# Performance work log

Measured on AMD Instinct MI355X. Metric: run time of the kernel, lower is better.

## Reference

```python
import jax, jax.numpy as jnp
import numpy as np

N, E, IN, H, C, T = 50000, 800000, 128, 64, 64, 2
F1, FO1 = H, H // T   # conv1: per-tower in/out feats
F2, FO2 = H, C // T   # conv2
STD_EPS = 1e-5
BN_EPS = 1e-5


def setup_inputs() -> dict:
    key = jax.random.key(0)
    ks = jax.random.split(key, 12)
    rn = lambda k, s, sc=0.05: jax.random.normal(k, s, jnp.float32) * sc
    return {
        "x": jax.random.normal(ks[0], (N, IN), jnp.float32),
        "embed_W": rn(ks[1], (IN, H)),
        "embed_b": jnp.zeros((H,), jnp.float32),
        "pre_W1": rn(ks[2], (T, 2 * F1, F1)),
        "pre_b1": jnp.zeros((T, F1), jnp.float32),
        "post_W1": rn(ks[3], (T, 13 * F1, FO1)),
        "post_b1": jnp.zeros((T, FO1), jnp.float32),
        "lin_W1": rn(ks[4], (H, H)),
        "lin_b1": jnp.zeros((H,), jnp.float32),
        "bn_gamma": jnp.ones((H,), jnp.float32),
        "bn_beta": jnp.zeros((H,), jnp.float32),
        "pre_W2": rn(ks[5], (T, 2 * F2, F2)),
        "pre_b2": jnp.zeros((T, F2), jnp.float32),
        "post_W2": rn(ks[6], (T, 13 * F2, FO2)),
        "post_b2": jnp.zeros((T, FO2), jnp.float32),
        "lin_W2": rn(ks[7], (C, C)),
        "lin_b2": jnp.zeros((C,), jnp.float32),
        "src": jax.random.randint(ks[8], (E,), 0, N, jnp.int32),
        "dst": jax.random.randint(ks[9], (E,), 0, N, jnp.int32),
    }


def _pna_conv(h, src, dst, deg_raw, degc, avg_log, preW, preb, postW, postb, linW, linb):
    # h: [N, F] node feats; messages flow src -> dst, aggregated at dst.
    m = jnp.concatenate([h[dst], h[src]], axis=-1)            # [E, 2F]  (cat[x_i, x_j])
    m = jnp.einsum('ef,tfg->etg', m, preW) + preb[None]       # [E, T, F] per-tower pre-NN
    seg = lambda v: jax.ops.segment_sum(v, dst, num_segments=N)
    cnt = degc[:, None, None]                                 # clamped degree >= 1
    has = (deg_raw > 0)[:, None, None]
    mean = seg(m) / cnt                                       # [N, T, F]
    mean_sq = seg(m * m) / cnt
    mn = jnp.where(has, jax.ops.segment_min(m, dst, num_segments=N), 0.0)
    mx = jnp.where(has, jax.ops.segment_max(m, dst, num_segments=N), 0.0)
    std = jnp.sqrt(jax.nn.relu(mean_sq - mean * mean) + STD_EPS)
    agg = jnp.concatenate([mean, mn, mx, std], axis=-1)       # [N, T, 4F]
    ld = jnp.log(degc + 1.0)[:, None, None]
    out = jnp.concatenate([agg, agg * (ld / avg_log), agg * (avg_log / ld)], axis=-1)  # [N, T, 12F]
    F = h.shape[-1]
    out = jnp.concatenate([jnp.broadcast_to(h[:, None, :], (N, T, F)), out], axis=-1)  # [N, T, 13F]
    out = jnp.einsum('ntf,tfg->ntg', out, postW) + postb[None]  # [N, T, FO] per-tower post-NN
    return out.reshape(N, -1) @ linW + linb                    # final mixing Linear(out, out)


def reference(x, embed_W, embed_b, pre_W1, pre_b1, post_W1, post_b1, lin_W1, lin_b1,
              bn_gamma, bn_beta, pre_W2, pre_b2, post_W2, post_b2, lin_W2, lin_b2,
              src, dst):
    deg_raw = jax.ops.segment_sum(jnp.ones((E,), jnp.float32), dst, num_segments=N)
    degc = jnp.maximum(deg_raw, 1.0)
    avg_log = jnp.mean(jnp.log(deg_raw + 1.0))  # avg_deg['log'] from the graph's degrees
    h = x @ embed_W + embed_b
    h = _pna_conv(h, src, dst, deg_raw, degc, avg_log,
                  pre_W1, pre_b1, post_W1, post_b1, lin_W1, lin_b1)
    mu = jnp.mean(h, axis=0)
    var = jnp.mean((h - mu) ** 2, axis=0)
    h = bn_gamma * (h - mu) / jnp.sqrt(var + BN_EPS) + bn_beta
    h = jax.nn.relu(h)  # dropout is identity in eval mode
    return _pna_conv(h, src, dst, deg_raw, degc, avg_log,
                     pre_W2, pre_b2, post_W2, post_b2, lin_W2, lin_b2)
```

## Files before the change

### kernel.cpp

```cpp
#include <hip/hip_runtime.h>

#define N_NODES 50000
#define E_EDGES 800000
#define IN_F    128
#define H_F     64
#define STD_EPS 1e-5f
#define BN_EPS  1e-5f

__global__ __launch_bounds__(256) void k_hist(const int* __restrict__ dst,
                                              int* __restrict__ deg) {
  int e = blockIdx.x * 256 + threadIdx.x;
  if (e < E_EDGES) atomicAdd(&deg[dst[e]], 1);
}

__global__ __launch_bounds__(256) void k_sumlog(const int* __restrict__ deg,
                                                float* __restrict__ scalars) {
  __shared__ float red[256];
  int i = blockIdx.x * 256 + threadIdx.x;
  float v = 0.f;
  if (i < N_NODES) v = logf((float)deg[i] + 1.0f);
  red[threadIdx.x] = v; __syncthreads();
  for (int s = 128; s > 0; s >>= 1) {
    if (threadIdx.x < s) red[threadIdx.x] += red[threadIdx.x + s];
    __syncthreads();
  }
  if (threadIdx.x == 0) atomicAdd(&scalars[0], red[0]);
}

__global__ __launch_bounds__(256) void k_scan_part(const int* __restrict__ deg,
                                                   int* __restrict__ partials) {
  __shared__ int red[256];
  int base = blockIdx.x * 1024;
  int s = 0;
  for (int j = threadIdx.x; j < 1024; j += 256) {
    int i = base + j;
    if (i < N_NODES) s += deg[i];
  }
  red[threadIdx.x] = s; __syncthreads();
  for (int st = 128; st > 0; st >>= 1) {
    if (threadIdx.x < st) red[threadIdx.x] += red[threadIdx.x + st];
    __syncthreads();
  }
  if (threadIdx.x == 0) partials[blockIdx.x] = red[0];
}

__global__ void k_scan_mid(int* __restrict__ partials, int nblk,
                           float* __restrict__ scalars) {
  if (threadIdx.x == 0) {
    int run = 0;
    for (int b = 0; b < nblk; b++) { int v = partials[b]; partials[b] = run; run += v; }
    scalars[1] = scalars[0] / (float)N_NODES;
  }
}

__global__ __launch_bounds__(256) void k_scan_final(const int* __restrict__ deg,
                                                    const int* __restrict__ partials,
                                                    int* __restrict__ row_ptr,
                                                    int* __restrict__ cursor) {
  __shared__ int ts[256];
  int base = blockIdx.x * 1024 + threadIdx.x * 4;
  int d[4]; int s = 0;
#pragma unroll
  for (int j = 0; j < 4; j++) {
    int i = base + j;
    d[j] = (i < N_NODES) ? deg[i] : 0;
    s += d[j];
  }
  ts[threadIdx.x] = s; __syncthreads();
  for (int off = 1; off < 256; off <<= 1) {
    int t = (threadIdx.x >= off) ? ts[threadIdx.x - off] : 0;
    __syncthreads();
    ts[threadIdx.x] += t;
    __syncthreads();
  }
  int excl = (threadIdx.x > 0) ? ts[threadIdx.x - 1] : 0;
  int run = partials[blockIdx.x] + excl;
#pragma unroll
  for (int j = 0; j < 4; j++) {
    int i = base + j;
    if (i < N_NODES) { row_ptr[i] = run; cursor[i] = run; run += d[j]; }
  }
  if (blockIdx.x == 0 && threadIdx.x == 0) row_ptr[N_NODES] = E_EDGES;
}

__global__ __launch_bounds__(256) void k_scatter(const int* __restrict__ src,
                                                 const int* __restrict__ dst,
                                                 int* __restrict__ cursor,
                                                 int* __restrict__ csr_src) {
  int e = blockIdx.x * 256 + threadIdx.x;
  if (e < E_EDGES) {
    int d = dst[e];
    int p = atomicAdd(&cursor[d], 1);
    csr_src[p] = src[e];
  }
}

__global__ __launch_bounds__(256) void k_embed(const float* __restrict__ x,
                                               const float* __restrict__ W,
                                               const float* __restrict__ bias,
                                               float* __restrict__ h) {
  __shared__ float sW[IN_F * 64];
  __shared__ float sx[IN_F * 20];
  for (int i = threadIdx.x; i < IN_F * 64; i += 256) sW[i] = W[i];
  int j = threadIdx.x & 63, ng = threadIdx.x >> 6;
  float bj = bias[j];
  for (int grp = blockIdx.x; grp < N_NODES / 16; grp += gridDim.x) {
    int n0 = grp * 16;
    __syncthreads();
    for (int idx = threadIdx.x; idx < 16 * IN_F; idx += 256) {
      int nl = idx >> 7, k = idx & 127;
      sx[k * 20 + nl] = x[(size_t)(n0 + nl) * IN_F + k];
    }
    __syncthreads();
    float a0 = bj, a1 = bj, a2 = bj, a3 = bj;
    const float* xp = &sx[ng * 4];
#pragma unroll 4
    for (int k = 0; k < IN_F; k++) {
      float4 xv = *(const float4*)&xp[k * 20];
      float w = sW[k * 64 + j];
      a0 = fmaf(xv.x, w, a0); a1 = fmaf(xv.y, w, a1);
      a2 = fmaf(xv.z, w, a2); a3 = fmaf(xv.w, w, a3);
    }
    size_t ob = (size_t)(n0 + ng * 4) * 64 + j;
    h[ob] = a0; h[ob + 64] = a1; h[ob + 128] = a2; h[ob + 192] = a3;
  }
}

template <bool BN>
__global__ __launch_bounds__(256) void k_preab(const float* __restrict__ hin,
                                               const float* __restrict__ preW,
                                               const float* __restrict__ preb,
                                               const float* __restrict__ bnscale,
                                               const float* __restrict__ bnshift,
                                               float* __restrict__ h2out,
                                               float* __restrict__ hA,
                                               float* __restrict__ hB) {
  __shared__ float sW[128 * 64];
  __shared__ float sh[64 * 20];
  int t = blockIdx.x & 1;
  const float* Wsrc = preW + (size_t)t * 128 * 64;
  for (int i = threadIdx.x; i < 128 * 64; i += 256) sW[i] = Wsrc[i];
  int f = threadIdx.x & 63, ng = threadIdx.x >> 6;
  float pb = preb[t * 64 + f];
  const float* wA = &sW[f];
  const float* wB = &sW[64 * 64 + f];
  int nblk2 = gridDim.x >> 1;
  for (int grp = blockIdx.x >> 1; grp < N_NODES / 16; grp += nblk2) {
    int n0 = grp * 16;
    __syncthreads();
    for (int idx = threadIdx.x; idx < 16 * 64; idx += 256) {
      int nl = idx >> 6, k = idx & 63;
      float v = hin[(size_t)(n0 + nl) * 64 + k];
      if (BN) {
        v = fmaxf(fmaf(v, bnscale[k], bnshift[k]), 0.f);
        if (t == 0) h2out[(size_t)(n0 + nl) * 64 + k] = v;
      }
      sh[k * 20 + nl] = v;
    }
    __syncthreads();
    float a0 = pb, a1 = pb, a2 = pb, a3 = pb;
    float b0 = 0, b1 = 0, b2 = 0, b3 = 0;
    const float* hp = &sh[ng * 4];
#pragma unroll 4
    for (int k = 0; k < 64; k++) {
      float4 hv = *(const float4*)&hp[k * 20];
      float wa = wA[k * 64], wb = wB[k * 64];
      a0 = fmaf(hv.x, wa, a0); a1 = fmaf(hv.y, wa, a1);
      a2 = fmaf(hv.z, wa, a2); a3 = fmaf(hv.w, wa, a3);
      b0 = fmaf(hv.x, wb, b0); b1 = fmaf(hv.y, wb, b1);
      b2 = fmaf(hv.z, wb, b2); b3 = fmaf(hv.w, wb, b3);
    }
    size_t nb = (size_t)(n0 + ng * 4);
    int tf = t * 64 + f;
    hA[nb * 128 + tf] = a0;          hB[nb * 128 + tf] = b0;
    hA[(nb + 1) * 128 + tf] = a1;    hB[(nb + 1) * 128 + tf] = b1;
    hA[(nb + 2) * 128 + tf] = a2;    hB[(nb + 2) * 128 + tf] = b2;
    hA[(nb + 3) * 128 + tf] = a3;    hB[(nb + 3) * 128 + tf] = b3;
  }
}

__global__ __launch_bounds__(256, 6) void k_conv(const float* __restrict__ hA,
                                                 const float* __restrict__ hB,
                                                 const float* __restrict__ hskip,
                                                 const int* __restrict__ row_ptr,
                                                 const int* __restrict__ csr_src,
                                                 const float* __restrict__ postW,
                                                 const float* __restrict__ postb,
                                                 const float* __restrict__ linW,
                                                 const float* __restrict__ linb,
                                                 const float* __restrict__ scalars,
                                                 float* __restrict__ out) {
  __shared__ float sm[2 * 5 * 8 * 64];
  __shared__ float sAB[16];
  int w = threadIdx.x >> 6, lane = threadIdx.x & 63;
  int n0 = blockIdx.x * 8;
  int t = lane >> 5, fb = (lane & 31) * 2;
  int off = t * 64 + fb;
  float avg = scalars[1];

#pragma unroll 1
  for (int k = 0; k < 2; k++) {
    int nl = w * 2 + k;
    int n = n0 + nl;
    float2 a = *(const float2*)&hA[(size_t)n * 128 + off];
    int rp0 = __builtin_amdgcn_readfirstlane(row_ptr[n]);
    int rp1 = __builtin_amdgcn_readfirstlane(row_ptr[n + 1]);
    float sx0=0,sy0=0,qx0=0,qy0=0, sx1=0,sy1=0,qx1=0,qy1=0;
    float mnx0=INFINITY,mny0=INFINITY,mxx0=-INFINITY,mxy0=-INFINITY;
    float mnx1=INFINITY,mny1=INFINITY,mxx1=-INFINITY,mxy1=-INFINITY;
    int i = rp0;
    int end4 = rp0 + ((rp1 - rp0) & ~3);
    if (i < end4) {
      int s0 = csr_src[i], s1 = csr_src[i+1], s2 = csr_src[i+2], s3 = csr_src[i+3];
      while (true) {
        float2 v0 = *(const float2*)&hB[(size_t)s0 * 128 + off];
        float2 v1 = *(const float2*)&hB[(size_t)s1 * 128 + off];
        float2 v2 = *(const float2*)&hB[(size_t)s2 * 128 + off];
        float2 v3 = *(const float2*)&hB[(size_t)s3 * 128 + off];
        i += 4;
        bool more = (i < end4);
        if (more) { s0 = csr_src[i]; s1 = csr_src[i+1]; s2 = csr_src[i+2]; s3 = csr_src[i+3]; }
        float e0x = v0.x + a.x, e0y = v0.y + a.y;
        float e1x = v1.x + a.x, e1y = v1.y + a.y;
        float e2x = v2.x + a.x, e2y = v2.y + a.y;
        float e3x = v3.x + a.x, e3y = v3.y + a.y;
        sx0 += e0x; qx0 = fmaf(e0x,e0x,qx0); mnx0 = fminf(mnx0,e0x); mxx0 = fmaxf(mxx0,e0x);
        sy0 += e0y; qy0 = fmaf(e0y,e0y,qy0); mny0 = fminf(mny0,e0y); mxy0 = fmaxf(mxy0,e0y);
        sx1 += e1x; qx1 = fmaf(e1x,e1x,qx1); mnx1 = fminf(mnx1,e1x); mxx1 = fmaxf(mxx1,e1x);
        sy1 += e1y; qy1 = fmaf(e1y,e1y,qy1); mny1 = fminf(mny1,e1y); mxy1 = fmaxf(mxy1,e1y);
        sx0 += e2x; qx0 = fmaf(e2x,e2x,qx0); mnx0 = fminf(mnx0,e2x); mxx0 = fmaxf(mxx0,e2x);
        sy0 += e2y; qy0 = fmaf(e2y,e2y,qy0); mny0 = fminf(mny0,e2y); mxy0 = fmaxf(mxy0,e2y);
        sx1 += e3x; qx1 = fmaf(e3x,e3x,qx1); mnx1 = fminf(mnx1,e3x); mxx1 = fmaxf(mxx1,e3x);
        sy1 += e3y; qy1 = fmaf(e3y,e3y,qy1); mny1 = fminf(mny1,e3y); mxy1 = fmaxf(mxy1,e3y);
        if (!more) break;
      }
    }
    {
      int r = rp1 - i;
      if (r > 0) {
        int e1i = (r > 1) ? i + 1 : i;
        int e2i = (r > 2) ? i + 2 : i;
        int t0 = csr_src[i], t1 = csr_src[e1i], t2 = csr_src[e2i];
        float2 u0 = *(const float2*)&hB[(size_t)t0 * 128 + off];
        float2 u1 = *(const float2*)&hB[(size_t)t1 * 128 + off];
        float2 u2 = *(const float2*)&hB[(size_t)t2 * 128 + off];
        float ex = u0.x + a.x, ey = u0.y + a.y;
        sx0 += ex; qx0 = fmaf(ex,ex,qx0); mnx0 = fminf(mnx0,ex); mxx0 = fmaxf(mxx0,ex);
        sy0 += ey; qy0 = fmaf(ey,ey,qy0); mny0 = fminf(mny0,ey); mxy0 = fmaxf(mxy0,ey);
        if (r > 1) {
          ex = u1.x + a.x; ey = u1.y + a.y;
          sx1 += ex; qx1 = fmaf(ex,ex,qx1); mnx1 = fminf(mnx1,ex); mxx1 = fmaxf(mxx1,ex);
          sy1 += ey; qy1 = fmaf(ey,ey,qy1); mny1 = fminf(mny1,ey); mxy1 = fmaxf(mxy1,ey);
        }
        if (r > 2) {
          ex = u2.x + a.x; ey = u2.y + a.y;
          sx0 += ex; qx0 = fmaf(ex,ex,qx0); mnx0 = fminf(mnx0,ex); mxx0 = fmaxf(mxx0,ex);
          sy0 += ey; qy0 = fmaf(ey,ey,qy0); mny0 = fminf(mny0,ey); mxy0 = fmaxf(mxy0,ey);
        }
      }
    }
    int dg = rp1 - rp0;
    float cnt = (float)(dg > 0 ? dg : 1);
    float inv = 1.0f / cnt;
    float meanx = (sx0 + sx1) * inv, meany = (sy0 + sy1) * inv;
    float qx = qx0 + qx1, qy = qy0 + qy1;
    float sdx = sqrtf(fmaxf(qx * inv - meanx * meanx, 0.f) + STD_EPS);
    float sdy = sqrtf(fmaxf(qy * inv - meany * meany, 0.f) + STD_EPS);
    float mnx = fminf(mnx0, mnx1), mny = fminf(mny0, mny1);
    float mxx = fmaxf(mxx0, mxx1), mxy = fmaxf(mxy0, mxy1);
    if (dg == 0) { mnx = 0; mny = 0; mxx = 0; mxy = 0; }
    float ldv = logf(cnt + 1.f);
    float2 hsv = *(const float2*)&hskip[(size_t)n * 64 + fb];
    float* bp = &sm[t * 2560 + nl * 64 + fb];
    *(float2*)&bp[0]    = hsv;
    *(float2*)&bp[512]  = make_float2(meanx, meany);
    *(float2*)&bp[1024] = make_float2(mnx, mny);
    *(float2*)&bp[1536] = make_float2(mxx, mxy);
    *(float2*)&bp[2048] = make_float2(sdx, sdy);
    if (lane == 0) { sAB[nl] = ldv / avg; sAB[8 + nl] = avg / ldv; }
  }
  __syncthreads();

  float g1[8] = {0,0,0,0,0,0,0,0};
  float g2[8] = {0,0,0,0,0,0,0,0};
  float g3[8] = {0,0,0,0,0,0,0,0};
  {
    int g = lane & 31, hf0 = w * 16;
    const float* pw = &postW[(size_t)t * (832 * 32) + g];
    const float* vb = &sm[t * 2560 + hf0];
#pragma unroll
    for (int j = 0; j < 16; j += 4) {
      int f13 = hf0 + j;
      float w0 = pw[f13 * 32],       w1 = pw[(f13 + 1) * 32];
      float w2 = pw[(f13 + 2) * 32], w3 = pw[(f13 + 3) * 32];
#pragma unroll
      for (int nn = 0; nn < 8; nn++) {
        float4 v = *(const float4*)&vb[nn * 64 + j];
        g1[nn] = fmaf(v.w, w3, fmaf(v.z, w2, fmaf(v.y, w1, fmaf(v.x, w0, g1[nn]))));
      }
    }
#pragma unroll
    for (int fa = 0; fa < 4; fa++) {
      const float* vfa = &vb[(1 + fa) * 512];
#pragma unroll
      for (int j = 0; j < 16; j += 4) {
        int f13 = 64 + fa * 64 + hf0 + j;
        float w10 = pw[f13 * 32],         w11 = pw[(f13 + 1) * 32];
        float w12 = pw[(f13 + 2) * 32],   w13 = pw[(f13 + 3) * 32];
        float w20 = pw[(f13 + 256) * 32], w21 = pw[(f13 + 257) * 32];
        float w22 = pw[(f13 + 258) * 32], w23 = pw[(f13 + 259) * 32];
        float w30 = pw[(f13 + 512) * 32], w31 = pw[(f13 + 513) * 32];
        float w32 = pw[(f13 + 514) * 32], w33 = pw[(f13 + 515) * 32];
#pragma unroll
        for (int nn = 0; nn < 8; nn++) {
          float4 v = *(const float4*)&vfa[nn * 64 + j];
          g1[nn] = fmaf(v.w, w13, fmaf(v.z, w12, fmaf(v.y, w11, fmaf(v.x, w10, g1[nn]))));
          g2[nn] = fmaf(v.w, w23, fmaf(v.z, w22, fmaf(v.y, w21, fmaf(v.x, w20, g2[nn]))));
          g3[nn] = fmaf(v.w, w33, fmaf(v.z, w32, fmaf(v.y, w31, fmaf(v.x, w30, g3[nn]))));
        }
      }
    }
  }
  float o8[8];
#pragma unroll
  for (int nn = 0; nn < 8; nn++)
    o8[nn] = fmaf(sAB[8 + nn], g3[nn], fmaf(sAB[nn], g2[nn], g1[nn]));
  __syncthreads();

  {
    int sw = (w + (lane >> 4)) & 3;
#pragma unroll
    for (int nn = 0; nn < 8; nn++)
      sm[((nn * 64 + lane) << 2) + sw] = o8[nn];
  }
  __syncthreads();

  {
#pragma unroll
    for (int r = 0; r < 2; r++) {
      int idx = r * 256 + (int)threadIdx.x;
      float4 p = *(const float4*)&sm[idx << 2];
      sm[2048 + idx] = p.x + p.y + p.z + p.w + postb[idx & 63];
    }
  }
  __syncthreads();

  {
    float acc0 = linb[lane], acc1 = acc0;
    const float* lw = linW + lane;
    const float* p0 = &sm[2048 + (w * 2) * 64];
    const float* p1 = p0 + 64;
#pragma unroll
    for (int c = 0; c < 64; c += 4) {
      float lw0 = lw[c * 64], lw1 = lw[(c + 1) * 64];
      float lw2 = lw[(c + 2) * 64], lw3 = lw[(c + 3) * 64];
      float4 pa = *(const float4*)&p0[c];
      float4 pb2 = *(const float4*)&p1[c];
      acc0 = fmaf(pa.w, lw3, fmaf(pa.z, lw2, fmaf(pa.y, lw1, fmaf(pa.x, lw0, acc0))));
      acc1 = fmaf(pb2.w, lw3, fmaf(pb2.z, lw2, fmaf(pb2.y, lw1, fmaf(pb2.x, lw0, acc1))));
    }
    size_t ob = (size_t)(n0 + w * 2) * 64 + lane;
    out[ob] = acc0;
    out[ob + 64] = acc1;
  }
}

__global__ __launch_bounds__(256) void k_bnstats(const float* __restrict__ y,
                                                 float* __restrict__ bnsum,
                                                 float* __restrict__ bnsumsq) {
  __shared__ float r1[256], r2[256];
  int c = threadIdx.x & 63, r = threadIdx.x >> 6;
  float s = 0, q = 0;
  for (int n = blockIdx.x * 4 + r; n < N_NODES; n += gridDim.x * 4) {
    float v = y[(size_t)n * 64 + c];
    s += v; q = fmaf(v, v, q);
  }
  r1[threadIdx.x] = s; r2[threadIdx.x] = q; __syncthreads();
  if (threadIdx.x < 64) {
    s = r1[threadIdx.x] + r1[threadIdx.x + 64] + r1[threadIdx.x + 128] + r1[threadIdx.x + 192];
    q = r2[threadIdx.x] + r2[threadIdx.x + 64] + r2[threadIdx.x + 128] + r2[threadIdx.x + 192];
    atomicAdd(&bnsum[threadIdx.x], s);
    atomicAdd(&bnsumsq[threadIdx.x], q);
  }
}

__global__ void k_bnfin(const float* __restrict__ bnsum, const float* __restrict__ bnsumsq,
                        const float* __restrict__ gamma, const float* __restrict__ beta,
                        float* __restrict__ bnscale, float* __restrict__ bnshift) {
  int c = threadIdx.x;
  if (c < 64) {
    float mu = bnsum[c] * (1.f / N_NODES);
    float var = bnsumsq[c] * (1.f / N_NODES) - mu * mu;
    float sc = gamma[c] / sqrtf(var + BN_EPS);
    bnscale[c] = sc;
    bnshift[c] = fmaf(-mu, sc, beta[c]);
  }
}

extern "C" void kernel_launch(void* const* d_in, const int* in_sizes, int n_in,
                              void* d_out, int out_size, void* d_ws, size_t ws_size,
                              hipStream_t stream) {
  const float* x      = (const float*)d_in[0];
  const float* embW   = (const float*)d_in[1];
  const float* embB   = (const float*)d_in[2];
  const float* preW1  = (const float*)d_in[3];
  const float* preb1  = (const float*)d_in[4];
  const float* postW1 = (const float*)d_in[5];
  const float* postb1 = (const float*)d_in[6];
  const float* linW1  = (const float*)d_in[7];
  const float* linb1  = (const float*)d_in[8];
  const float* gamma  = (const float*)d_in[9];
  const float* beta   = (const float*)d_in[10];
  const float* preW2  = (const float*)d_in[11];
  const float* preb2  = (const float*)d_in[12];
  const float* postW2 = (const float*)d_in[13];
  const float* postb2 = (const float*)d_in[14];
  const float* linW2  = (const float*)d_in[15];
  const float* linb2  = (const float*)d_in[16];
  const int*   src    = (const int*)d_in[17];
  const int*   dst    = (const int*)d_in[18];
  float* out = (float*)d_out;

  char* w = (char*)d_ws;
  size_t o = 0;
  int*   deg     = (int*)(w + o);   o += (size_t)N_NODES * 4;
  float* scalars = (float*)(w + o); o += 64;
  float* bnsum   = (float*)(w + o); o += 256;
  float* bnsumsq = (float*)(w + o); o += 256;
  float* bnscale = (float*)(w + o); o += 256;
  float* bnshift = (float*)(w + o); o += 256;
  size_t zero_len = o;
  o = (o + 255) & ~(size_t)255;
  int* partials = (int*)(w + o);  o += 256;
  int* row_ptr  = (int*)(w + o);  o += (size_t)(N_NODES + 1) * 4; o = (o + 255) & ~(size_t)255;
  int* cursor   = (int*)(w + o);  o += (size_t)N_NODES * 4;       o = (o + 255) & ~(size_t)255;
  int* csr      = (int*)(w + o);  o += (size_t)E_EDGES * 4;       o = (o + 255) & ~(size_t)255;
  float* h1 = (float*)(w + o); o += (size_t)N_NODES * 64 * 4;
  float* y1 = (float*)(w + o); o += (size_t)N_NODES * 64 * 4;
  float* h2 = (float*)(w + o); o += (size_t)N_NODES * 64 * 4;
  float* hA = (float*)(w + o); o += (size_t)N_NODES * 128 * 4;
  float* hB = (float*)(w + o); o += (size_t)N_NODES * 128 * 4;

  hipMemsetAsync(w, 0, zero_len, stream);

  const int NBLK_SCAN = (N_NODES + 1023) / 1024;
  k_hist<<<(E_EDGES + 255) / 256, 256, 0, stream>>>(dst, deg);
  k_sumlog<<<(N_NODES + 255) / 256, 256, 0, stream>>>(deg, scalars);
  k_scan_part<<<NBLK_SCAN, 256, 0, stream>>>(deg, partials);
  k_scan_mid<<<1, 64, 0, stream>>>(partials, NBLK_SCAN, scalars);
  k_scan_final<<<NBLK_SCAN, 256, 0, stream>>>(deg, partials, row_ptr, cursor);
  k_scatter<<<(E_EDGES + 255) / 256, 256, 0, stream>>>(src, dst, cursor, csr);

  k_embed<<<768, 256, 0, stream>>>(x, embW, embB, h1);

  k_preab<false><<<1024, 256, 0, stream>>>(h1, preW1, preb1, nullptr, nullptr, nullptr, hA, hB);
  k_conv<<<N_NODES / 8, 256, 0, stream>>>(hA, hB, h1, row_ptr, csr,
                                          postW1, postb1, linW1, linb1, scalars, y1);
  k_bnstats<<<256, 256, 0, stream>>>(y1, bnsum, bnsumsq);
  k_bnfin<<<1, 64, 0, stream>>>(bnsum, bnsumsq, gamma, beta, bnscale, bnshift);

  k_preab<true><<<1024, 256, 0, stream>>>(y1, preW2, preb2, bnscale, bnshift, h2, hA, hB);
  k_conv<<<N_NODES / 8, 256, 0, stream>>>(hA, hB, h2, row_ptr, csr,
                                          postW2, postb2, linW2, linb2, scalars, out);
}
```

Measured before the change: 580.8 us.

## Fuse log-degree sum into scan, enlarge preab node tile, tune launch bounds

Folds the log-degree reduction into the scan partial kernel, which removes one launch and one pass over the degree array. Reworks k_preab so each thread computes 8 nodes instead of 4, with the A/B weights interleaved into float2 pairs in shared memory. This gives more register reuse per weight load, adds bounds checks and a smaller grid of 768 blocks. Raises the k_conv occupancy hint from 6 to 7 blocks per CU, which may increase register pressure or spilling.

```diff
diff --git a/kernel.cpp b/kernel.cpp
--- a/kernel.cpp
+++ b/kernel.cpp
@@ -13,35 +13,29 @@
   if (e < E_EDGES) atomicAdd(&deg[dst[e]], 1);
 }
 
-__global__ __launch_bounds__(256) void k_sumlog(const int* __restrict__ deg,
-                                                float* __restrict__ scalars) {
-  __shared__ float red[256];
-  int i = blockIdx.x * 256 + threadIdx.x;
-  float v = 0.f;
-  if (i < N_NODES) v = logf((float)deg[i] + 1.0f);
-  red[threadIdx.x] = v; __syncthreads();
-  for (int s = 128; s > 0; s >>= 1) {
-    if (threadIdx.x < s) red[threadIdx.x] += red[threadIdx.x + s];
-    __syncthreads();
-  }
-  if (threadIdx.x == 0) atomicAdd(&scalars[0], red[0]);
-}
-
 __global__ __launch_bounds__(256) void k_scan_part(const int* __restrict__ deg,
-                                                   int* __restrict__ partials) {
+                                                   int* __restrict__ partials,
+                                                   float* __restrict__ scalars) {
   __shared__ int red[256];
+  __shared__ float redf[256];
   int base = blockIdx.x * 1024;
-  int s = 0;
+  int s = 0; float ls = 0.f;
   for (int j = threadIdx.x; j < 1024; j += 256) {
     int i = base + j;
-    if (i < N_NODES) s += deg[i];
-  }
-  red[threadIdx.x] = s; __syncthreads();
+    if (i < N_NODES) { int d = deg[i]; s += d; ls += logf((float)d + 1.0f); }
+  }
+  red[threadIdx.x] = s; redf[threadIdx.x] = ls; __syncthreads();
   for (int st = 128; st > 0; st >>= 1) {
-    if (threadIdx.x < st) red[threadIdx.x] += red[threadIdx.x + st];
-    __syncthreads();
-  }
-  if (threadIdx.x == 0) partials[blockIdx.x] = red[0];
+    if (threadIdx.x < st) {
+      red[threadIdx.x] += red[threadIdx.x + st];
+      redf[threadIdx.x] += redf[threadIdx.x + st];
+    }
+    __syncthreads();
+  }
+  if (threadIdx.x == 0) {
+    partials[blockIdx.x] = red[0];
+    atomicAdd(&scalars[0], redf[0]);
+  }
 }
 
 __global__ void k_scan_mid(int* __restrict__ partials, int nblk,
@@ -135,51 +129,68 @@
                                                float* __restrict__ h2out,
                                                float* __restrict__ hA,
                                                float* __restrict__ hB) {
-  __shared__ float sW[128 * 64];
-  __shared__ float sh[64 * 20];
+  __shared__ float sWp[64 * 128];
+  __shared__ float sh[64 * 36];
   int t = blockIdx.x & 1;
   const float* Wsrc = preW + (size_t)t * 128 * 64;
-  for (int i = threadIdx.x; i < 128 * 64; i += 256) sW[i] = Wsrc[i];
+  for (int i = threadIdx.x; i < 64 * 64; i += 256) {
+    int k = i >> 6, f = i & 63;
+    float wa = Wsrc[k * 64 + f];
+    float wb = Wsrc[(64 + k) * 64 + f];
+    *(float2*)&sWp[k * 128 + f * 2] = make_float2(wa, wb);
+  }
   int f = threadIdx.x & 63, ng = threadIdx.x >> 6;
   float pb = preb[t * 64 + f];
-  const float* wA = &sW[f];
-  const float* wB = &sW[64 * 64 + f];
   int nblk2 = gridDim.x >> 1;
-  for (int grp = blockIdx.x >> 1; grp < N_NODES / 16; grp += nblk2) {
-    int n0 = grp * 16;
-    __syncthreads();
-    for (int idx = threadIdx.x; idx < 16 * 64; idx += 256) {
+  const int NGRP = (N_NODES + 31) / 32;
+  for (int grp = blockIdx.x >> 1; grp < NGRP; grp += nblk2) {
+    int n0 = grp * 32;
+    __syncthreads();
+    for (int idx = threadIdx.x; idx < 32 * 64; idx += 256) {
       int nl = idx >> 6, k = idx & 63;
-      float v = hin[(size_t)(n0 + nl) * 64 + k];
-      if (BN) {
-        v = fmaxf(fmaf(v, bnscale[k], bnshift[k]), 0.f);
-        if (t == 0) h2out[(size_t)(n0 + nl) * 64 + k] = v;
-      }
-      sh[k * 20 + nl] = v;
-    }
-    __syncthreads();
-    float a0 = pb, a1 = pb, a2 = pb, a3 = pb;
-    float b0 = 0, b1 = 0, b2 = 0, b3 = 0;
-    const float* hp = &sh[ng * 4];
+      int n = n0 + nl;
+      float v = 0.f;
+      if (n < N_NODES) {
+        v = hin[(size_t)n * 64 + k];
+        if (BN) {
+          v = fmaxf(fmaf(v, bnscale[k], bnshift[k]), 0.f);
+          if (t == 0) h2out[(size_t)n * 64 + k] = v;
+        }
+      }
+      sh[k * 36 + nl] = v;
+    }
+    __syncthreads();
+    float a[8] = {pb, pb, pb, pb, pb, pb, pb, pb};
+    float b[8] = {0, 0, 0, 0, 0, 0, 0, 0};
+    const float* hp = &sh[ng * 8];
+    const float* wp = &sWp[f * 2];
 #pragma unroll 4
     for (int k = 0; k < 64; k++) {
-      float4 hv = *(const float4*)&hp[k * 20];
-      float wa = wA[k * 64], wb = wB[k * 64];
-      a0 = fmaf(hv.x, wa, a0); a1 = fmaf(hv.y, wa, a1);
-      a2 = fmaf(hv.z, wa, a2); a3 = fmaf(hv.w, wa, a3);
-      b0 = fmaf(hv.x, wb, b0); b1 = fmaf(hv.y, wb, b1);
-      b2 = fmaf(hv.z, wb, b2); b3 = fmaf(hv.w, wb, b3);
-    }
-    size_t nb = (size_t)(n0 + ng * 4);
+      float4 h0 = *(const float4*)&hp[k * 36];
+      float4 h1 = *(const float4*)&hp[k * 36 + 4];
+      float2 w2 = *(const float2*)&wp[k * 128];
+      a[0] = fmaf(h0.x, w2.x, a[0]); b[0] = fmaf(h0.x, w2.y, b[0]);
+      a[1] = fmaf(h0.y, w2.x, a[1]); b[1] = fmaf(h0.y, w2.y, b[1]);
+      a[2] = fmaf(h0.z, w2.x, a[2]); b[2] = fmaf(h0.z, w2.y, b[2]);
+      a[3] = fmaf(h0.w, w2.x, a[3]); b[3] = fmaf(h0.w, w2.y, b[3]);
+      a[4] = fmaf(h1.x, w2.x, a[4]); b[4] = fmaf(h1.x, w2.y, b[4]);
+      a[5] = fmaf(h1.y, w2.x, a[5]); b[5] = fmaf(h1.y, w2.y, b[5]);
+      a[6] = fmaf(h1.z, w2.x, a[6]); b[6] = fmaf(h1.z, w2.y, b[6]);
+      a[7] = fmaf(h1.w, w2.x, a[7]); b[7] = fmaf(h1.w, w2.y, b[7]);
+    }
     int tf = t * 64 + f;
-    hA[nb * 128 + tf] = a0;          hB[nb * 128 + tf] = b0;
-    hA[(nb + 1) * 128 + tf] = a1;    hB[(nb + 1) * 128 + tf] = b1;
-    hA[(nb + 2) * 128 + tf] = a2;    hB[(nb + 2) * 128 + tf] = b2;
-    hA[(nb + 3) * 128 + tf] = a3;    hB[(nb + 3) * 128 + tf] = b3;
-  }
-}
-
-__global__ __launch_bounds__(256, 6) void k_conv(const float* __restrict__ hA,
+#pragma unroll
+    for (int j = 0; j < 8; j++) {
+      int n = n0 + ng * 8 + j;
+      if (n < N_NODES) {
+        hA[(size_t)n * 128 + tf] = a[j];
+        hB[(size_t)n * 128 + tf] = b[j];
+      }
+    }
+  }
+}
+
+__global__ __launch_bounds__(256, 7) void k_conv(const float* __restrict__ hA,
                                                  const float* __restrict__ hB,
                                                  const float* __restrict__ hskip,
                                                  const int* __restrict__ row_ptr,
@@ -445,21 +456,20 @@
 
   const int NBLK_SCAN = (N_NODES + 1023) / 1024;
   k_hist<<<(E_EDGES + 255) / 256, 256, 0, stream>>>(dst, deg);
-  k_sumlog<<<(N_NODES + 255) / 256, 256, 0, stream>>>(deg, scalars);
-  k_scan_part<<<NBLK_SCAN, 256, 0, stream>>>(deg, partials);
+  k_scan_part<<<NBLK_SCAN, 256, 0, stream>>>(deg, partials, scalars);
   k_scan_mid<<<1, 64, 0, stream>>>(partials, NBLK_SCAN, scalars);
   k_scan_final<<<NBLK_SCAN, 256, 0, stream>>>(deg, partials, row_ptr, cursor);
   k_scatter<<<(E_EDGES + 255) / 256, 256, 0, stream>>>(src, dst, cursor, csr);
 
   k_embed<<<768, 256, 0, stream>>>(x, embW, embB, h1);
 
-  k_preab<false><<<1024, 256, 0, stream>>>(h1, preW1, preb1, nullptr, nullptr, nullptr, hA, hB);
+  k_preab<false><<<768, 256, 0, stream>>>(h1, preW1, preb1, nullptr, nullptr, nullptr, hA, hB);
   k_conv<<<N_NODES / 8, 256, 0, stream>>>(hA, hB, h1, row_ptr, csr,
                                           postW1, postb1, linW1, linb1, scalars, y1);
   k_bnstats<<<256, 256, 0, stream>>>(y1, bnsum, bnsumsq);
   k_bnfin<<<1, 64, 0, stream>>>(bnsum, bnsumsq, gamma, beta, bnscale, bnshift);
 
-  k_preab<true><<<1024, 256, 0, stream>>>(y1, preW2, preb2, bnscale, bnshift, h2, hA, hB);
+  k_preab<true><<<768, 256, 0, stream>>>(y1, preW2, preb2, bnscale, bnshift, h2, hA, hB);
   k_conv<<<N_NODES / 8, 256, 0, stream>>>(hA, hB, h2, row_ptr, csr,
                                           postW2, postb2, linW2, linb2, scalars, out);
 }
```

Result: faster. 553.5 us (-4.7%).
